# Performance work log

Hardware: AMD Instinct MI355X
Metric: run time of the kernel (lower is better)

Reference implementation:

```python
import jax, jax.numpy as jnp
import numpy as np

UNITS = 128
D_FEAT = 128
B, N = 4, 4096
EDGE_PROB = 0.01  # avg in-degree ~ N * EDGE_PROB ~ 41


def setup_inputs() -> dict:
    key = jax.random.key(0)
    k1, k2, k3, k4 = jax.random.split(key, 4)
    x = jax.random.normal(k1, (B, N, D_FEAT), dtype=jnp.float32)
    # binary adjacency mask, as consumed by tf.where(adj)
    adj = (jax.random.uniform(k2, (B, N, N)) < EDGE_PROB).astype(jnp.float32)
    # Dense(units, use_bias=False) kernels: msg on concat(x_snd, x_rec) -> [2d, U];
    # node_update on concat(x, messages) -> [d+U, U]
    W_msg = (jax.random.normal(k3, (2 * D_FEAT, UNITS), dtype=jnp.float32)
             / np.sqrt(2 * D_FEAT).astype(np.float32))
    W_upd = (jax.random.normal(k4, (D_FEAT + UNITS, UNITS), dtype=jnp.float32)
             / np.sqrt(D_FEAT + UNITS).astype(np.float32))
    return {"x": x, "adj": adj, "W_msg": W_msg, "W_upd": W_upd}


def reference(x, adj, W_msg, W_upd):
    # Faithful to MPNN2.call: edges are (b, s, r) where adj[b, s, r] != 0.
    # message per edge = concat(x[b,s], x[b,r]) @ W_msg = x[b,s]@Ws + x[b,r]@Wr.
    # messages[b,r] = segment_mean over incoming edges. Since the receiver term
    # x[b,r]@Wr is identical for all edges into r, its mean is itself, and the
    # sender term's mean is (adj^T @ (x@Ws)) / in_degree. Empty segments -> 0
    # (tf.math.unsorted_segment_mean semantics). This avoids data-dependent
    # edge-list shapes and is jit-compatible.
    d = x.shape[-1]
    Ws, Wr = W_msg[:d], W_msg[d:]          # [d, U] each
    xs = x @ Ws                            # sender contribution  [B, N, U]
    xr = x @ Wr                            # receiver contribution [B, N, U]
    deg = jnp.einsum('bsr->br', adj)[..., None]          # in-degree [B, N, 1]
    snd_sum = jnp.einsum('bsr,bsu->bru', adj, xs)        # [B, N, U]
    messages = jnp.where(deg > 0,
                         snd_sum / jnp.maximum(deg, 1.0) + xr,
                         0.0)
    # node_update on concat(x, messages); activation=None, use_bias=False
    return jnp.concatenate([x, messages], axis=-1) @ W_upd
```

## Files before the change

### kernel.cpp

```cpp
#include <hip/hip_runtime.h>
#include <hip/hip_bf16.h>

#define BB 4
#define NN 4096
#define DF 128
#define ROWS (BB*NN)
#define CAP 128

__device__ __forceinline__ float bf2f(unsigned short u) {
    union { unsigned int i; float f; } cv; cv.i = ((unsigned int)u) << 16; return cv.f;
}
__device__ __forceinline__ unsigned short f2bf(float f) {
    union { float f; unsigned int i; } cv; cv.f = f;
    unsigned int i = cv.i;
    return (unsigned short)((i + 0x7FFFu + ((i >> 16) & 1u)) >> 16);
}

__global__ __launch_bounds__(256) void scan_adj(const float* __restrict__ adj,
                                                int* __restrict__ cnt,
                                                int* __restrict__ bucket) {
    int tid = blockIdx.x * 256 + threadIdx.x;
    float4 v = ((const float4*)adj)[tid];
    int e = tid << 2;
    int b = e >> 24;
    int s = (e >> 12) & 4095;
    int rgbase = (b << 12) | (e & 4095);
    float vals[4] = {v.x, v.y, v.z, v.w};
#pragma unroll
    for (int k = 0; k < 4; ++k) {
        if (vals[k] != 0.0f) {
            int rg = rgbase + k;
            int slot = atomicAdd(&cnt[rg], 1);
            if (slot < CAP) bucket[rg * CAP + slot] = s;
        }
    }
}

__global__ __launch_bounds__(128) void fold_weights(const float* __restrict__ Wmsg,
                                                    const float* __restrict__ Wupd,
                                                    float* __restrict__ Wcat) {
    __shared__ float ldsS[128], ldsR[128];
    int k = blockIdx.x, t = threadIdx.x;
    ldsS[t] = Wmsg[k * 128 + t];
    ldsR[t] = Wmsg[(128 + k) * 128 + t];
    __syncthreads();
    float a1 = 0.f, a2 = 0.f;
#pragma unroll 8
    for (int m = 0; m < 128; ++m) {
        float wu = Wupd[(128 + m) * 128 + t];
        a1 += ldsS[m] * wu;
        a2 += ldsR[m] * wu;
    }
    Wcat[k * 384 + t]       = Wupd[k * 128 + t];
    Wcat[k * 384 + 128 + t] = a2;
    Wcat[k * 384 + 256 + t] = a1;
}

#define BM 64
#define BK 64
#define BN 128
__global__ __launch_bounds__(256) void gemm_x_wcat(const float* __restrict__ X,
                                                   const float* __restrict__ Wcat,
                                                   float* __restrict__ T1,
                                                   float* __restrict__ D2,
                                                   unsigned short* __restrict__ YB) {
    __shared__ float As[BM][68];
    __shared__ float Bs[BK][BN];
    int t  = threadIdx.x;
    int m0 = blockIdx.x * BM;
    int nb = blockIdx.y;
    int n0 = nb * BN;
    int cn = t & 15;
    int cm = t >> 4;

    float acc[4][8];
#pragma unroll
    for (int i = 0; i < 4; ++i)
#pragma unroll
        for (int j = 0; j < 8; ++j) acc[i][j] = 0.f;

    for (int c = 0; c < 2; ++c) {
#pragma unroll
        for (int i = 0; i < 4; ++i) {
            int f = t + 256 * i;
            int m = f >> 4, k4 = f & 15;
            float4 v = *(const float4*)(X + (size_t)(m0 + m) * 128 + c * 64 + k4 * 4);
            *(float4*)(&As[m][k4 * 4]) = v;
        }
#pragma unroll
        for (int i = 0; i < 8; ++i) {
            int f = t + 256 * i;
            int k = f >> 5, n4 = f & 31;
            float4 v = *(const float4*)(Wcat + (size_t)(c * 64 + k) * 384 + n0 + n4 * 4);
            *(float4*)(&Bs[k][n4 * 4]) = v;
        }
        __syncthreads();
#pragma unroll 8
        for (int kk = 0; kk < BK; ++kk) {
            float av[4];
#pragma unroll
            for (int i = 0; i < 4; ++i) av[i] = As[cm * 4 + i][kk];
            float4 b0 = *(float4*)(&Bs[kk][cn * 8]);
            float4 b1 = *(float4*)(&Bs[kk][cn * 8 + 4]);
            float bv[8] = {b0.x, b0.y, b0.z, b0.w, b1.x, b1.y, b1.z, b1.w};
#pragma unroll
            for (int i = 0; i < 4; ++i)
#pragma unroll
                for (int j = 0; j < 8; ++j) acc[i][j] += av[i] * bv[j];
        }
        __syncthreads();
    }
#pragma unroll
    for (int i = 0; i < 4; ++i) {
        int row = m0 + cm * 4 + i;
        if (nb == 2) {
            uint4 o;
            o.x = (unsigned)f2bf(acc[i][0]) | ((unsigned)f2bf(acc[i][1]) << 16);
            o.y = (unsigned)f2bf(acc[i][2]) | ((unsigned)f2bf(acc[i][3]) << 16);
            o.z = (unsigned)f2bf(acc[i][4]) | ((unsigned)f2bf(acc[i][5]) << 16);
            o.w = (unsigned)f2bf(acc[i][6]) | ((unsigned)f2bf(acc[i][7]) << 16);
            *(uint4*)(YB + (size_t)row * 128 + cn * 8) = o;
        } else {
            float* dst = (nb == 0 ? T1 : D2) + (size_t)row * 128 + cn * 8;
            float4 o0 = {acc[i][0], acc[i][1], acc[i][2], acc[i][3]};
            float4 o1 = {acc[i][4], acc[i][5], acc[i][6], acc[i][7]};
            *(float4*)(dst)     = o0;
            *(float4*)(dst + 4) = o1;
        }
    }
}

__global__ __launch_bounds__(256) void gather_out(const float* __restrict__ T1,
                                                  const float* __restrict__ D2,
                                                  const unsigned short* __restrict__ YB,
                                                  const int* __restrict__ cnt,
                                                  const int* __restrict__ bucket,
                                                  float* __restrict__ out) {
    __shared__ int lds_s[2][CAP];
    int t = threadIdx.x;
    int sub = t >> 7, j = t & 127;
    int rg = blockIdx.x * 2 + sub;
    int c = cnt[rg];
    if (c > CAP) c = CAP;
    if (j < c) lds_s[sub][j] = bucket[rg * CAP + j];
    __syncthreads();
    float t1 = T1[(size_t)rg * 128 + j];
    float res = t1;
    if (c > 0) {
        int b = rg >> 12;
        const unsigned short* yb = YB + ((size_t)(b << 12)) * 128 + j;
        float a0 = 0.f, a1 = 0.f, a2 = 0.f, a3 = 0.f;
        int e = 0;
        for (; e + 4 <= c; e += 4) {
            int s0 = lds_s[sub][e + 0];
            int s1 = lds_s[sub][e + 1];
            int s2 = lds_s[sub][e + 2];
            int s3 = lds_s[sub][e + 3];
            unsigned short u0 = yb[(size_t)s0 * 128];
            unsigned short u1 = yb[(size_t)s1 * 128];
            unsigned short u2 = yb[(size_t)s2 * 128];
            unsigned short u3 = yb[(size_t)s3 * 128];
            a0 += bf2f(u0); a1 += bf2f(u1); a2 += bf2f(u2); a3 += bf2f(u3);
        }
        for (; e < c; ++e) a0 += bf2f(yb[(size_t)lds_s[sub][e] * 128]);
        res = t1 + D2[(size_t)rg * 128 + j] + (a0 + a1 + a2 + a3) * (1.0f / (float)c);
    }
    out[(size_t)rg * 128 + j] = res;
}

extern "C" void kernel_launch(void* const* d_in, const int* in_sizes, int n_in,
                              void* d_out, int out_size, void* d_ws, size_t ws_size,
                              hipStream_t stream) {
    const float* x    = (const float*)d_in[0];
    const float* adj  = (const float*)d_in[1];
    const float* Wmsg = (const float*)d_in[2];
    const float* Wupd = (const float*)d_in[3];
    float* out = (float*)d_out;

    char* ws = (char*)d_ws;
    float*          Wcat   = (float*)(ws);
    float*          T1     = (float*)(ws + 262144);
    float*          D2     = (float*)(ws + 262144 + 8388608);
    unsigned short* YB     = (unsigned short*)(ws + 262144 + 2*8388608);
    int*            cntb   = (int*)(ws + 262144 + 2*8388608 + 4194304);
    int*            bucket = (int*)(ws + 262144 + 2*8388608 + 4194304 + 65536);

    hipMemsetAsync(cntb, 0, ROWS * sizeof(int), stream);

    scan_adj<<<(BB * NN * NN) / 4 / 256, 256, 0, stream>>>(adj, cntb, bucket);
    fold_weights<<<128, 128, 0, stream>>>(Wmsg, Wupd, Wcat);
    gemm_x_wcat<<<dim3(ROWS / BM, 3), 256, 0, stream>>>(x, Wcat, T1, D2, YB);
    gather_out<<<ROWS / 2, 256, 0, stream>>>(T1, D2, YB, cntb, bucket, out);
}
```

Measured before the change: 442.5 us.

## Replace global-atomic adjacency scan with LDS-counted chunked buckets and vectorized gather

The adjacency scan now gives each block a tile of 256 receivers by 512 senders. It counts edges with LDS atomics and writes per-chunk buckets plus per-chunk counts, which removes the global memset and the contended global atomics. The gather reads the chunked buckets, compacts them in LDS, and processes two output columns per thread with packed bf16 loads. T1 and D2 are interleaved into one buffer. The per-chunk cap of 32 could drop edges for dense rows, and scan parallelism falls to 512 blocks.

```diff
diff --git a/kernel.cpp b/kernel.cpp
--- a/kernel.cpp
+++ b/kernel.cpp
@@ -3,12 +3,15 @@
 
 #define BB 4
 #define NN 4096
-#define DF 128
 #define ROWS (BB*NN)
-#define CAP 128
-
-__device__ __forceinline__ float bf2f(unsigned short u) {
-    union { unsigned int i; float f; } cv; cv.i = ((unsigned int)u) << 16; return cv.f;
+#define RT 256
+#define SC 512
+#define NCH (NN/SC)
+#define CAPC 32
+#define BSTRIDE (NCH*CAPC)
+
+__device__ __forceinline__ float asf(unsigned int u) {
+    union { unsigned int i; float f; } cv; cv.i = u; return cv.f;
 }
 __device__ __forceinline__ unsigned short f2bf(float f) {
     union { float f; unsigned int i; } cv; cv.f = f;
@@ -16,24 +19,39 @@
     return (unsigned short)((i + 0x7FFFu + ((i >> 16) & 1u)) >> 16);
 }
 
-__global__ __launch_bounds__(256) void scan_adj(const float* __restrict__ adj,
-                                                int* __restrict__ cnt,
-                                                int* __restrict__ bucket) {
-    int tid = blockIdx.x * 256 + threadIdx.x;
-    float4 v = ((const float4*)adj)[tid];
-    int e = tid << 2;
-    int b = e >> 24;
-    int s = (e >> 12) & 4095;
-    int rgbase = (b << 12) | (e & 4095);
-    float vals[4] = {v.x, v.y, v.z, v.w};
-#pragma unroll
-    for (int k = 0; k < 4; ++k) {
-        if (vals[k] != 0.0f) {
-            int rg = rgbase + k;
-            int slot = atomicAdd(&cnt[rg], 1);
-            if (slot < CAP) bucket[rg * CAP + slot] = s;
-        }
-    }
+__global__ __launch_bounds__(256) void scan_bucket(const float* __restrict__ adj,
+                                                   int* __restrict__ cnt2,
+                                                   int* __restrict__ bucket) {
+    __shared__ int lcnt[RT];
+    int bI = blockIdx.x;
+    int rt = bI & 15;
+    int ch = (bI >> 4) & 7;
+    int b  = bI >> 7;
+    int r0 = rt * RT;
+    int s0 = ch * SC;
+    int t  = threadIdx.x;
+    lcnt[t] = 0;
+    __syncthreads();
+    int cg = t & 63;
+    int sl = t >> 6;
+    const float* base = adj + ((size_t)b * NN + s0) * NN + r0 + cg * 4;
+    for (int k = 0; k < SC / 4; ++k) {
+        int srow = k * 4 + sl;
+        float4 v = *(const float4*)(base + (size_t)srow * NN);
+        int s = s0 + srow;
+        float vals[4] = {v.x, v.y, v.z, v.w};
+#pragma unroll
+        for (int j = 0; j < 4; ++j) {
+            if (vals[j] != 0.0f) {
+                int col = cg * 4 + j;
+                int slot = atomicAdd(&lcnt[col], 1);
+                if (slot < CAPC)
+                    bucket[(size_t)((b << 12) + r0 + col) * BSTRIDE + ch * CAPC + slot] = s;
+            }
+        }
+    }
+    __syncthreads();
+    cnt2[(size_t)((b << 12) + r0 + t) * NCH + ch] = lcnt[t];
 }
 
 __global__ __launch_bounds__(128) void fold_weights(const float* __restrict__ Wmsg,
@@ -61,8 +79,7 @@
 #define BN 128
 __global__ __launch_bounds__(256) void gemm_x_wcat(const float* __restrict__ X,
                                                    const float* __restrict__ Wcat,
-                                                   float* __restrict__ T1,
-                                                   float* __restrict__ D2,
+                                                   float* __restrict__ TD,
                                                    unsigned short* __restrict__ YB) {
     __shared__ float As[BM][68];
     __shared__ float Bs[BK][BN];
@@ -121,7 +138,7 @@
             o.w = (unsigned)f2bf(acc[i][6]) | ((unsigned)f2bf(acc[i][7]) << 16);
             *(uint4*)(YB + (size_t)row * 128 + cn * 8) = o;
         } else {
-            float* dst = (nb == 0 ? T1 : D2) + (size_t)row * 128 + cn * 8;
+            float* dst = TD + (size_t)row * 256 + nb * 128 + cn * 8;
             float4 o0 = {acc[i][0], acc[i][1], acc[i][2], acc[i][3]};
             float4 o1 = {acc[i][4], acc[i][5], acc[i][6], acc[i][7]};
             *(float4*)(dst)     = o0;
@@ -130,42 +147,69 @@
     }
 }
 
-__global__ __launch_bounds__(256) void gather_out(const float* __restrict__ T1,
-                                                  const float* __restrict__ D2,
-                                                  const unsigned short* __restrict__ YB,
-                                                  const int* __restrict__ cnt,
+__global__ __launch_bounds__(256) void gather_out(const float* __restrict__ TD,
+                                                  const unsigned int* __restrict__ YB,
+                                                  const int* __restrict__ cnt2,
                                                   const int* __restrict__ bucket,
                                                   float* __restrict__ out) {
-    __shared__ int lds_s[2][CAP];
-    int t = threadIdx.x;
-    int sub = t >> 7, j = t & 127;
-    int rg = blockIdx.x * 2 + sub;
-    int c = cnt[rg];
-    if (c > CAP) c = CAP;
-    if (j < c) lds_s[sub][j] = bucket[rg * CAP + j];
-    __syncthreads();
-    float t1 = T1[(size_t)rg * 128 + j];
-    float res = t1;
-    if (c > 0) {
+    __shared__ int lds_s[4][BSTRIDE];
+    int t  = threadIdx.x;
+    int rs = t >> 6;
+    int j2 = t & 63;
+    int rg = blockIdx.x * 4 + rs;
+
+    int c[NCH];
+    int ctot = 0, deg = 0;
+    int pre[NCH];
+#pragma unroll
+    for (int ch = 0; ch < NCH; ++ch) {
+        c[ch] = cnt2[(size_t)rg * NCH + ch];
+        deg += c[ch];
+        int cc = min(c[ch], CAPC);
+        pre[ch] = ctot;
+        ctot += cc;
+    }
+#pragma unroll
+    for (int ch = 0; ch < NCH; ++ch) {
+        int cc = min(c[ch], CAPC);
+        if (j2 < cc)
+            lds_s[rs][pre[ch] + j2] = bucket[(size_t)rg * BSTRIDE + ch * CAPC + j2];
+    }
+    __syncthreads();
+
+    const float2* td = (const float2*)(TD + (size_t)rg * 256);
+    float2 t1 = td[j2];
+    float2 res = t1;
+    if (deg > 0) {
         int b = rg >> 12;
-        const unsigned short* yb = YB + ((size_t)(b << 12)) * 128 + j;
-        float a0 = 0.f, a1 = 0.f, a2 = 0.f, a3 = 0.f;
+        const unsigned int* yb = YB + (((size_t)b << 12)) * 64 + j2;
+        float al0 = 0.f, ah0 = 0.f, al1 = 0.f, ah1 = 0.f;
+        float al2 = 0.f, ah2 = 0.f, al3 = 0.f, ah3 = 0.f;
         int e = 0;
-        for (; e + 4 <= c; e += 4) {
-            int s0 = lds_s[sub][e + 0];
-            int s1 = lds_s[sub][e + 1];
-            int s2 = lds_s[sub][e + 2];
-            int s3 = lds_s[sub][e + 3];
-            unsigned short u0 = yb[(size_t)s0 * 128];
-            unsigned short u1 = yb[(size_t)s1 * 128];
-            unsigned short u2 = yb[(size_t)s2 * 128];
-            unsigned short u3 = yb[(size_t)s3 * 128];
-            a0 += bf2f(u0); a1 += bf2f(u1); a2 += bf2f(u2); a3 += bf2f(u3);
-        }
-        for (; e < c; ++e) a0 += bf2f(yb[(size_t)lds_s[sub][e] * 128]);
-        res = t1 + D2[(size_t)rg * 128 + j] + (a0 + a1 + a2 + a3) * (1.0f / (float)c);
-    }
-    out[(size_t)rg * 128 + j] = res;
+        for (; e + 4 <= ctot; e += 4) {
+            int s0 = lds_s[rs][e + 0];
+            int s1 = lds_s[rs][e + 1];
+            int s2 = lds_s[rs][e + 2];
+            int s3 = lds_s[rs][e + 3];
+            unsigned u0 = yb[(size_t)s0 * 64];
+            unsigned u1 = yb[(size_t)s1 * 64];
+            unsigned u2 = yb[(size_t)s2 * 64];
+            unsigned u3 = yb[(size_t)s3 * 64];
+            al0 += asf(u0 << 16); ah0 += asf(u0 & 0xffff0000u);
+            al1 += asf(u1 << 16); ah1 += asf(u1 & 0xffff0000u);
+            al2 += asf(u2 << 16); ah2 += asf(u2 & 0xffff0000u);
+            al3 += asf(u3 << 16); ah3 += asf(u3 & 0xffff0000u);
+        }
+        for (; e < ctot; ++e) {
+            unsigned u = yb[(size_t)lds_s[rs][e] * 64];
+            al0 += asf(u << 16); ah0 += asf(u & 0xffff0000u);
+        }
+        float inv = 1.0f / (float)deg;
+        float2 d2 = td[64 + j2];
+        res.x = t1.x + d2.x + (al0 + al1 + al2 + al3) * inv;
+        res.y = t1.y + d2.y + (ah0 + ah1 + ah2 + ah3) * inv;
+    }
+    ((float2*)(out + (size_t)rg * 128))[j2] = res;
 }
 
 extern "C" void kernel_launch(void* const* d_in, const int* in_sizes, int n_in,
@@ -179,16 +223,13 @@
 
     char* ws = (char*)d_ws;
     float*          Wcat   = (float*)(ws);
-    float*          T1     = (float*)(ws + 262144);
-    float*          D2     = (float*)(ws + 262144 + 8388608);
-    unsigned short* YB     = (unsigned short*)(ws + 262144 + 2*8388608);
-    int*            cntb   = (int*)(ws + 262144 + 2*8388608 + 4194304);
-    int*            bucket = (int*)(ws + 262144 + 2*8388608 + 4194304 + 65536);
-
-    hipMemsetAsync(cntb, 0, ROWS * sizeof(int), stream);
-
-    scan_adj<<<(BB * NN * NN) / 4 / 256, 256, 0, stream>>>(adj, cntb, bucket);
+    float*          TD     = (float*)(ws + 262144);
+    unsigned short* YB     = (unsigned short*)(ws + 262144 + 16777216);
+    int*            cnt2   = (int*)(ws + 262144 + 16777216 + 4194304);
+    int*            bucket = (int*)(ws + 262144 + 16777216 + 4194304 + 524288);
+
+    scan_bucket<<<512, 256, 0, stream>>>(adj, cnt2, bucket);
     fold_weights<<<128, 128, 0, stream>>>(Wmsg, Wupd, Wcat);
-    gemm_x_wcat<<<dim3(ROWS / BM, 3), 256, 0, stream>>>(x, Wcat, T1, D2, YB);
-    gather_out<<<ROWS / 2, 256, 0, stream>>>(T1, D2, YB, cntb, bucket, out);
-}
+    gemm_x_wcat<<<dim3(ROWS / BM, 3), 256, 0, stream>>>(x, Wcat, TD, YB);
+    gather_out<<<ROWS / 4, 256, 0, stream>>>(TD, (const unsigned int*)YB, cnt2, bucket, out);
+}
```

Measured after the change: 462.8 us. 1.05x slower.
